# Optimization experiments

Hardware: AMD Instinct MI355X
Metric: run time of the kernel (lower is better)

The kernel has to match this reference:

```python
import jax, jax.numpy as jnp
import numpy as np

N, D, R, E = 20000, 256, 12, 200000  # nodes, feat dim, relation labels, edges


def setup_inputs() -> dict:
    key = jax.random.key(0)
    ks = jax.random.split(key, 8)
    x = jax.random.normal(ks[0], (N, D), dtype=jnp.float32)
    dep_idx = jax.random.randint(ks[1], (E,), 0, N)
    rel_idx = jax.random.randint(ks[2], (E,), 0, R)
    gov_idx = jax.random.randint(ks[3], (E,), 0, N)
    # nn.Linear params: W is [out,in], y = x @ W.T + b
    W_self = jax.random.normal(ks[4], (D, D), dtype=jnp.float32) * 0.02
    b_self = jnp.zeros((D,), dtype=jnp.float32)
    # 2R relation weights: [0..R) forward labels, [R..2R) reversed '_r' labels
    W_rel = jax.random.normal(ks[5], (2 * R, D, D), dtype=jnp.float32) * 0.02
    b_rel = jax.random.normal(ks[6], (2 * R, D), dtype=jnp.float32) * 0.02
    return {"x": x, "dep_idx": dep_idx, "rel_idx": rel_idx, "gov_idx": gov_idx,
            "W_self": W_self, "b_self": b_self, "W_rel": W_rel, "b_rel": b_rel}


def reference(x, dep_idx, rel_idx, gov_idx, W_self, b_self, W_rel, b_rel):
    R_ = W_rel.shape[0] // 2
    # self transform for every node
    out = x @ W_self.T + b_self  # [N, D]
    # all-relation transform, grouped GEMM instead of per-edge Linear calls
    T = jnp.einsum('nd,rod->nro', x, W_rel)  # [N, 2R, D]
    # forward edges: dependent += W[rel] @ x[governor] + b[rel]
    msg_f = T[gov_idx, rel_idx] + b_rel[rel_idx]          # [E, D]
    # reverse edges: governor += W[rel_r] @ x[dependent] + b[rel_r]
    msg_r = T[dep_idx, rel_idx + R_] + b_rel[rel_idx + R_]  # [E, D]
    out = out.at[dep_idx].add(msg_f).at[gov_idx].add(msg_r)
    return jax.nn.relu(out)
```

## Files before the change

### kernel.cpp

```cpp
#include <hip/hip_runtime.h>
#include <cstdint>
#include <cstddef>

#define DD 256
#define NSLOT 25
#define SELFSLOT 12

typedef unsigned short u16;
typedef __bf16 bf16t;
typedef bf16t bf16x8 __attribute__((ext_vector_type(8)));
typedef unsigned short us8 __attribute__((ext_vector_type(8)));
typedef unsigned short us4 __attribute__((ext_vector_type(4)));
typedef float f32x4 __attribute__((ext_vector_type(4)));

__device__ __forceinline__ u16 f2bf(float f) {
    uint32_t u = __builtin_bit_cast(uint32_t, f);
    u += 0x7FFFu + ((u >> 16) & 1u);
    return (u16)(u >> 16);
}
__device__ __forceinline__ float bf2f(u16 h) {
    uint32_t u = ((uint32_t)h) << 16;
    return __builtin_bit_cast(float, u);
}

__global__ void k_convert_all(const float* __restrict__ x, const float* __restrict__ W_rel,
                              const float* __restrict__ W_self, const float* __restrict__ b_self,
                              const float* __restrict__ b_rel,
                              u16* __restrict__ xb, u16* __restrict__ Wb,
                              float* __restrict__ ba, int NDD) {
    const int s0 = NDD;
    const int s1 = s0 + 12 * 65536;
    const int s2 = s1 + 65536;
    const int s3 = s2 + 12 * 65536;
    const int s4 = s3 + NSLOT * DD;
    int i = blockIdx.x * blockDim.x + threadIdx.x;
    int st = gridDim.x * blockDim.x;
    for (; i < s4; i += st) {
        if (i < s0) {
            xb[i] = f2bf(x[i]);
        } else if (i < s1) {
            int k = i - s0; Wb[k] = f2bf(W_rel[k]);
        } else if (i < s2) {
            int k = i - s1; Wb[12 * 65536 + k] = f2bf(W_self[k]);
        } else if (i < s3) {
            int k = i - s2; Wb[13 * 65536 + k] = f2bf(W_rel[12 * 65536 + k]);
        } else {
            int k = i - s3;
            float v;
            if (k < 12 * DD) v = b_rel[k];
            else if (k < 13 * DD) v = b_self[k - 12 * DD];
            else v = b_rel[k - DD];
            ba[k] = v;
        }
    }
}

__global__ void k_markhist(const int* __restrict__ dep, const int* __restrict__ rel,
                           const int* __restrict__ gov, int E, int N, int SG,
                           int* __restrict__ flag, int* __restrict__ bcnt) {
    int i = blockIdx.x * blockDim.x + threadIdx.x;
    int st = gridDim.x * blockDim.x;
    for (int j = i; j < E; j += st) {
        int r = rel[j], d = dep[j], g = gov[j];
        flag[r * N + g] = 1;
        flag[(13 + r) * N + d] = 1;
        atomicAdd(&bcnt[(r / SG) * N + d], 1);
        atomicAdd(&bcnt[((13 + r) / SG) * N + g], 1);
    }
    for (int j = i; j < N; j += st) flag[SELFSLOT * N + j] = 1;
}

__global__ void k_scan1d(const int* __restrict__ A, int* __restrict__ outA,
                         int* __restrict__ bsumA, int lenA, int nbA,
                         const int* __restrict__ B, int* __restrict__ outB,
                         int* __restrict__ bsumB, int lenB) {
    __shared__ int sm[256];
    const int* in; int* outp; int* bs; int len; int lb;
    if ((int)blockIdx.x < nbA) { in = A; outp = outA; bs = bsumA; len = lenA; lb = blockIdx.x; }
    else { in = B; outp = outB; bs = bsumB; len = lenB; lb = blockIdx.x - nbA; }
    int tid = threadIdx.x;
    int i = lb * 256 + tid;
    int v = (i < len) ? in[i] : 0;
    sm[tid] = v;
    __syncthreads();
    for (int off = 1; off < 256; off <<= 1) {
        int t = (tid >= off) ? sm[tid - off] : 0;
        __syncthreads();
        sm[tid] += t;
        __syncthreads();
    }
    if (i < len) outp[i] = sm[tid] - v;
    if (tid == 255) bs[lb] = sm[255];
}

__global__ void k_scan2d(const int* __restrict__ bsumA, int* __restrict__ bbasA, int nbA,
                         const int* __restrict__ bsumB, int* __restrict__ bbasB, int nbB) {
    __shared__ int sm[256];
    int t = threadIdx.x;
    for (int which = 0; which < 2; ++which) {
        const int* bsum = which ? bsumB : bsumA;
        int* bbase = which ? bbasB : bbasA;
        int nb = which ? nbB : nbA;
        int pre[8];
        int tot = 0;
        for (int j = 0; j < 8; ++j) {
            int idx = t * 8 + j;
            int v = (idx < nb) ? bsum[idx] : 0;
            pre[j] = tot;
            tot += v;
        }
        sm[t] = tot;
        __syncthreads();
        for (int off = 1; off < 256; off <<= 1) {
            int x = (t >= off) ? sm[t - off] : 0;
            __syncthreads();
            sm[t] += x;
            __syncthreads();
        }
        int base = sm[t] - tot;
        for (int j = 0; j < 8; ++j) {
            int idx = t * 8 + j;
            if (idx < nb) bbase[idx] = base + pre[j];
        }
        __syncthreads();
    }
}

__global__ void k_scan3d(int* __restrict__ pos, const int* __restrict__ bbasA,
                         const int* __restrict__ flag, int NN, int N,
                         int* __restrict__ rksrc,
                         int* __restrict__ bcsr, int* __restrict__ bcur,
                         const int* __restrict__ bbasB, int B2, int E2) {
    int i = blockIdx.x * 256 + threadIdx.x;
    if (i < NN) {
        int v = pos[i] + bbasA[i >> 8];
        pos[i] = v;
        if (i == NN - 1) pos[NN] = v + flag[i];
        if (flag[i]) {
            int slot = i / N;
            rksrc[v] = i - slot * N;
        }
    }
    if (i < B2) {
        int v = bcsr[i] + bbasB[i >> 8];
        bcsr[i] = v;
        bcur[i] = v;
    }
    if (i == 0) bcsr[B2] = E2;
}

__global__ void k_scatter(const int* __restrict__ dep, const int* __restrict__ rel,
                          const int* __restrict__ gov, int E, int N, int SG,
                          const int* __restrict__ pos,
                          int* __restrict__ cursor, int* __restrict__ epay) {
    int i = blockIdx.x * blockDim.x + threadIdx.x;
    int st = gridDim.x * blockDim.x;
    for (; i < E; i += st) {
        int r = rel[i], d = dep[i], g = gov[i];
        int g0 = r / SG;
        int p = atomicAdd(&cursor[g0 * N + d], 1);
        epay[p] = pos[r * N + g] - pos[g0 * SG * N];
        int gs = 13 + r;
        int g1 = gs / SG;
        int q = atomicAdd(&cursor[g1 * N + g], 1);
        epay[q] = pos[gs * N + d] - pos[g1 * SG * N];
    }
}

__global__ __launch_bounds__(256, 4) void k_T(
    const u16* __restrict__ xb, const u16* __restrict__ Wb, const float* __restrict__ ba,
    const int* __restrict__ pos, const int* __restrict__ rksrc, u16* __restrict__ T,
    int N, int gslot0, int Sg) {
    __shared__ u16 sm[2 * 128 * 72];
    __shared__ int s_src[128];
    u16 (*As)[72] = (u16(*)[72])sm;
    u16 (*Bs)[72] = (u16(*)[72])(sm + 128 * 72);

    const int bx = blockIdx.x;
    const int mtile = bx / (2 * Sg);
    const int rem = bx - mtile * 2 * Sg;
    const int slot = rem >> 1;
    const int n0 = (rem & 1) * 128;
    const int gslot = gslot0 + slot;
    const int u0 = pos[gslot * N];
    const int used = pos[(gslot + 1) * N] - u0;
    const int row0 = mtile * 128;
    if (row0 >= used) return;
    const int gbase = pos[gslot0 * N];
    const int tid = threadIdx.x;

    if (tid < 128) {
        int r = row0 + tid;
        s_src[tid] = rksrc[u0 + ((r < used) ? r : (used - 1))];
    }
    __syncthreads();

    const int lane = tid & 63, wv = tid >> 6;
    const int wr = wv & 1, wc = wv >> 1;
    const int l15 = lane & 15, quad = lane >> 4;
    const int srow = tid >> 1, sh = (tid & 1) * 32;
    const u16* bgp = Wb + ((size_t)gslot << 16) + (size_t)(n0 + srow) * DD + sh;

    f32x4 acc[4][4] = {};
    for (int kb = 0; kb < DD; kb += 64) {
        {
            const us8* ga = (const us8*)(xb + (size_t)s_src[srow] * DD + kb + sh);
            us8 a0 = ga[0], a1 = ga[1], a2 = ga[2], a3 = ga[3];
            *(us8*)&As[srow][sh]      = a0;
            *(us8*)&As[srow][sh + 8]  = a1;
            *(us8*)&As[srow][sh + 16] = a2;
            *(us8*)&As[srow][sh + 24] = a3;
            const us8* gb = (const us8*)(bgp + kb);
            us8 b0 = gb[0], b1 = gb[1], b2 = gb[2], b3 = gb[3];
            *(us8*)&Bs[srow][sh]      = b0;
            *(us8*)&Bs[srow][sh + 8]  = b1;
            *(us8*)&Bs[srow][sh + 16] = b2;
            *(us8*)&Bs[srow][sh + 24] = b3;
        }
        __syncthreads();
        #pragma unroll
        for (int ks = 0; ks < 2; ++ks) {
            const int kk = ks * 32 + quad * 8;
            bf16x8 af[4], bfv[4];
            #pragma unroll
            for (int mt = 0; mt < 4; ++mt)
                af[mt] = __builtin_bit_cast(bf16x8, *(const us8*)&As[wr * 64 + mt * 16 + l15][kk]);
            #pragma unroll
            for (int nt = 0; nt < 4; ++nt)
                bfv[nt] = __builtin_bit_cast(bf16x8, *(const us8*)&Bs[wc * 64 + nt * 16 + l15][kk]);
            #pragma unroll
            for (int mt = 0; mt < 4; ++mt)
                #pragma unroll
                for (int nt = 0; nt < 4; ++nt)
                    acc[mt][nt] = __builtin_amdgcn_mfma_f32_16x16x32_bf16(
                        af[mt], bfv[nt], acc[mt][nt], 0, 0, 0);
        }
        __syncthreads();
    }

    float bv[4];
    #pragma unroll
    for (int nt = 0; nt < 4; ++nt) bv[nt] = ba[gslot * DD + n0 + wc * 64 + nt * 16 + l15];
    u16* trb = sm + wv * (64 * 72);
    #pragma unroll
    for (int nt = 0; nt < 4; ++nt)
        #pragma unroll
        for (int mt = 0; mt < 4; ++mt)
            #pragma unroll
            for (int j = 0; j < 4; ++j)
                trb[(mt * 16 + quad * 4 + j) * 72 + nt * 16 + l15] =
                    f2bf(acc[mt][nt][j] + bv[nt]);
    __syncthreads();
    const int trow0 = u0 - gbase + row0 + wr * 64;
    const int half = lane & 1;
    #pragma unroll
    for (int it = 0; it < 2; ++it) {
        int r = it * 32 + (lane >> 1);
        if (row0 + wr * 64 + r < used) {
            const us8* sp = (const us8*)(trb + r * 72 + half * 32);
            us8 v0 = sp[0], v1 = sp[1], v2 = sp[2], v3 = sp[3];
            us8* dp = (us8*)(T + (size_t)(trow0 + r) * DD + n0 + wc * 64 + half * 32);
            dp[0] = v0; dp[1] = v1; dp[2] = v2; dp[3] = v3;
        }
    }
}

__global__ __launch_bounds__(256) void k_gather(
    const u16* __restrict__ T, const int* __restrict__ epay,
    const int* __restrict__ csr, const int* __restrict__ pos,
    float* __restrict__ out, int N, int bktBase, int selfKeyBase, int gfN,
    int first, int last) {
    int wid = (blockIdx.x * 256 + threadIdx.x) >> 6;
    if (wid >= N) return;
    int feat = (threadIdx.x & 63) * 4;
    f32x4 a = {0.0f, 0.0f, 0.0f, 0.0f};
    if (!first) a = *(const f32x4*)(out + (size_t)wid * DD + feat);
    if (selfKeyBase >= 0) {
        int p = pos[selfKeyBase + wid] - pos[gfN];
        us4 v = *(const us4*)(T + (size_t)p * DD + feat);
        a[0] += bf2f(v[0]); a[1] += bf2f(v[1]); a[2] += bf2f(v[2]); a[3] += bf2f(v[3]);
    }
    int beg = csr[bktBase + wid], end = csr[bktBase + wid + 1];
    f32x4 b = {0, 0, 0, 0}, c = {0, 0, 0, 0}, d4 = {0, 0, 0, 0};
    int j = beg;
    for (; j + 3 < end; j += 4) {
        int p0 = epay[j], p1 = epay[j + 1], p2 = epay[j + 2], p3 = epay[j + 3];
        us4 v0 = *(const us4*)(T + (size_t)p0 * DD + feat);
        us4 v1 = *(const us4*)(T + (size_t)p1 * DD + feat);
        us4 v2 = *(const us4*)(T + (size_t)p2 * DD + feat);
        us4 v3 = *(const us4*)(T + (size_t)p3 * DD + feat);
        a[0] += bf2f(v0[0]); a[1] += bf2f(v0[1]); a[2] += bf2f(v0[2]); a[3] += bf2f(v0[3]);
        b[0] += bf2f(v1[0]); b[1] += bf2f(v1[1]); b[2] += bf2f(v1[2]); b[3] += bf2f(v1[3]);
        c[0] += bf2f(v2[0]); c[1] += bf2f(v2[1]); c[2] += bf2f(v2[2]); c[3] += bf2f(v2[3]);
        d4[0] += bf2f(v3[0]); d4[1] += bf2f(v3[1]); d4[2] += bf2f(v3[2]); d4[3] += bf2f(v3[3]);
    }
    for (; j < end; ++j) {
        int p0 = epay[j];
        us4 v0 = *(const us4*)(T + (size_t)p0 * DD + feat);
        a[0] += bf2f(v0[0]); a[1] += bf2f(v0[1]); a[2] += bf2f(v0[2]); a[3] += bf2f(v0[3]);
    }
    a[0] += b[0] + c[0] + d4[0];
    a[1] += b[1] + c[1] + d4[1];
    a[2] += b[2] + c[2] + d4[2];
    a[3] += b[3] + c[3] + d4[3];
    if (last) {
        a[0] = fmaxf(a[0], 0.0f); a[1] = fmaxf(a[1], 0.0f);
        a[2] = fmaxf(a[2], 0.0f); a[3] = fmaxf(a[3], 0.0f);
    }
    *(f32x4*)(out + (size_t)wid * DD + feat) = a;
}

extern "C" void kernel_launch(void* const* d_in, const int* in_sizes, int n_in,
                              void* d_out, int out_size, void* d_ws, size_t ws_size,
                              hipStream_t stream) {
    const float* x      = (const float*)d_in[0];
    const int*   dep    = (const int*)  d_in[1];
    const int*   rel    = (const int*)  d_in[2];
    const int*   gov    = (const int*)  d_in[3];
    const float* W_self = (const float*)d_in[4];
    const float* b_self = (const float*)d_in[5];
    const float* W_rel  = (const float*)d_in[6];
    const float* b_rel  = (const float*)d_in[7];
    float* out = (float*)d_out;

    const int N  = in_sizes[0] / DD;
    const int E  = in_sizes[1];
    const int NN = NSLOT * N;

    char* w = (char*)d_ws;
    auto alloc = [&](size_t bytes) {
        char* p = w;
        w += (bytes + 255) & ~(size_t)255;
        return p;
    };
    u16* xb    = (u16*)alloc((size_t)N * DD * sizeof(u16));
    u16* Wb    = (u16*)alloc((size_t)NSLOT * DD * DD * sizeof(u16));
    float* ba  = (float*)alloc((size_t)NSLOT * DD * sizeof(float));
    int* flag  = (int*)alloc((size_t)NN * sizeof(int));
    int* pos   = (int*)alloc(((size_t)NN + 1) * sizeof(int));
    int* rksrc = (int*)alloc(((size_t)2 * E + N) * sizeof(int));
    int* bcnt  = (int*)alloc((size_t)6 * N * sizeof(int));
    int* bcsr  = (int*)alloc(((size_t)6 * N + 1) * sizeof(int));
    int* bcur  = (int*)alloc((size_t)6 * N * sizeof(int));
    int* bsumA = (int*)alloc((size_t)2048 * sizeof(int));
    int* bbasA = (int*)alloc((size_t)2048 * sizeof(int));
    int* bsumB = (int*)alloc((size_t)2048 * sizeof(int));
    int* bbasB = (int*)alloc((size_t)2048 * sizeof(int));
    int* epay  = (int*)alloc((size_t)2 * E * sizeof(int));

    size_t used = (size_t)(w - (char*)d_ws);
    size_t avail = (ws_size > used) ? (ws_size - used) : 0;

    int NGROUP = 2, SG = 13;
    for (int ng = 1; ng <= 5; ++ng) {
        int sg = (NSLOT + ng - 1) / ng;
        size_t maxB = 0;
        for (int g = 0; g < ng; ++g) {
            int s0 = g * sg, s1 = s0 + sg; if (s1 > NSLOT) s1 = NSLOT;
            if (s0 >= NSLOT) break;
            int hasSelf = (s0 <= SELFSLOT && SELFSLOT < s1) ? 1 : 0;
            size_t rels = (size_t)(s1 - s0 - hasSelf);
            size_t rows = rels * N; if (rows > (size_t)2 * E) rows = (size_t)2 * E;
            rows += hasSelf ? (size_t)N : 0;
            if (rows > maxB) maxB = rows;
        }
        if (maxB * ((size_t)DD * 2) <= avail) { NGROUP = ng; SG = sg; break; }
        NGROUP = ng + 1; SG = (NSLOT + NGROUP - 1) / NGROUP;
    }
    u16* T = (u16*)w;
    const int B2 = NGROUP * N;

    k_convert_all<<<1024, 256, 0, stream>>>(x, W_rel, W_self, b_self, b_rel,
                                            xb, Wb, ba, N * DD);

    hipMemsetAsync(flag, 0, (size_t)NN * sizeof(int), stream);
    hipMemsetAsync(bcnt, 0, (size_t)B2 * sizeof(int), stream);
    k_markhist<<<512, 256, 0, stream>>>(dep, rel, gov, E, N, SG, flag, bcnt);

    const int nbA = (NN + 255) / 256;
    const int nbB = (B2 + 255) / 256;
    k_scan1d<<<nbA + nbB, 256, 0, stream>>>(flag, pos, bsumA, NN, nbA, bcnt, bcsr, bsumB, B2);
    k_scan2d<<<1, 256, 0, stream>>>(bsumA, bbasA, nbA, bsumB, bbasB, nbB);
    k_scan3d<<<nbA, 256, 0, stream>>>(pos, bbasA, flag, NN, N, rksrc, bcsr, bcur, bbasB, B2, 2 * E);

    k_scatter<<<(E + 255) / 256, 256, 0, stream>>>(dep, rel, gov, E, N, SG, pos, bcur, epay);

    const int tilesPerSlot = (N + 127) / 128;
    const int gBlocks = (N + 3) / 4;
    for (int g = 0; g < NGROUP; ++g) {
        int s0 = g * SG;
        if (s0 >= NSLOT) break;
        int Sg = NSLOT - s0; if (Sg > SG) Sg = SG;
        k_T<<<dim3(tilesPerSlot * Sg * 2), 256, 0, stream>>>(
            xb, Wb, ba, pos, rksrc, T, N, s0, Sg);
        int hasSelf = (s0 <= SELFSLOT && SELFSLOT < s0 + Sg);
        k_gather<<<gBlocks, 256, 0, stream>>>(
            T, epay, bcsr, pos, out, N, g * N,
            hasSelf ? SELFSLOT * N : -1, s0 * N,
            (g == 0) ? 1 : 0, (g == NGROUP - 1) ? 1 : 0);
    }
}
```

Before: 279.3 us.

## Fuse convert and histogram kernels; transpose MFMA epilogue for vector stores

```diff
diff --git a/kernel.cpp b/kernel.cpp
--- a/kernel.cpp
+++ b/kernel.cpp
@@ -23,51 +23,51 @@
     return __builtin_bit_cast(float, u);
 }
 
-__global__ void k_convert_all(const float* __restrict__ x, const float* __restrict__ W_rel,
-                              const float* __restrict__ W_self, const float* __restrict__ b_self,
-                              const float* __restrict__ b_rel,
-                              u16* __restrict__ xb, u16* __restrict__ Wb,
-                              float* __restrict__ ba, int NDD) {
-    const int s0 = NDD;
-    const int s1 = s0 + 12 * 65536;
-    const int s2 = s1 + 65536;
-    const int s3 = s2 + 12 * 65536;
-    const int s4 = s3 + NSLOT * DD;
-    int i = blockIdx.x * blockDim.x + threadIdx.x;
-    int st = gridDim.x * blockDim.x;
-    for (; i < s4; i += st) {
-        if (i < s0) {
-            xb[i] = f2bf(x[i]);
-        } else if (i < s1) {
-            int k = i - s0; Wb[k] = f2bf(W_rel[k]);
-        } else if (i < s2) {
-            int k = i - s1; Wb[12 * 65536 + k] = f2bf(W_self[k]);
-        } else if (i < s3) {
-            int k = i - s2; Wb[13 * 65536 + k] = f2bf(W_rel[12 * 65536 + k]);
-        } else {
-            int k = i - s3;
-            float v;
-            if (k < 12 * DD) v = b_rel[k];
-            else if (k < 13 * DD) v = b_self[k - 12 * DD];
-            else v = b_rel[k - DD];
-            ba[k] = v;
-        }
-    }
-}
-
-__global__ void k_markhist(const int* __restrict__ dep, const int* __restrict__ rel,
-                           const int* __restrict__ gov, int E, int N, int SG,
-                           int* __restrict__ flag, int* __restrict__ bcnt) {
-    int i = blockIdx.x * blockDim.x + threadIdx.x;
-    int st = gridDim.x * blockDim.x;
-    for (int j = i; j < E; j += st) {
-        int r = rel[j], d = dep[j], g = gov[j];
-        flag[r * N + g] = 1;
-        flag[(13 + r) * N + d] = 1;
-        atomicAdd(&bcnt[(r / SG) * N + d], 1);
-        atomicAdd(&bcnt[((13 + r) / SG) * N + g], 1);
-    }
-    for (int j = i; j < N; j += st) flag[SELFSLOT * N + j] = 1;
+__global__ void k_prep(const float* __restrict__ x, const float* __restrict__ W_rel,
+                       const float* __restrict__ W_self, const float* __restrict__ b_self,
+                       const float* __restrict__ b_rel,
+                       u16* __restrict__ xb, u16* __restrict__ Wb, float* __restrict__ ba,
+                       const int* __restrict__ dep, const int* __restrict__ rel,
+                       const int* __restrict__ gov, int E, int N, int SG,
+                       int* __restrict__ flag, int* __restrict__ bcnt, int NDD) {
+    if (blockIdx.x < 1024) {
+        const int s0 = NDD;
+        const int s1 = s0 + 12 * 65536;
+        const int s2 = s1 + 65536;
+        const int s3 = s2 + 12 * 65536;
+        const int s4 = s3 + NSLOT * DD;
+        int i = blockIdx.x * 256 + threadIdx.x;
+        int st = 1024 * 256;
+        for (; i < s4; i += st) {
+            if (i < s0) {
+                xb[i] = f2bf(x[i]);
+            } else if (i < s1) {
+                int k = i - s0; Wb[k] = f2bf(W_rel[k]);
+            } else if (i < s2) {
+                int k = i - s1; Wb[12 * 65536 + k] = f2bf(W_self[k]);
+            } else if (i < s3) {
+                int k = i - s2; Wb[13 * 65536 + k] = f2bf(W_rel[12 * 65536 + k]);
+            } else {
+                int k = i - s3;
+                float v;
+                if (k < 12 * DD) v = b_rel[k];
+                else if (k < 13 * DD) v = b_self[k - 12 * DD];
+                else v = b_rel[k - DD];
+                ba[k] = v;
+            }
+        }
+    } else {
+        int i = (blockIdx.x - 1024) * 256 + threadIdx.x;
+        int st = 512 * 256;
+        for (int j = i; j < E; j += st) {
+            int r = rel[j], d = dep[j], g = gov[j];
+            flag[r * N + g] = 1;
+            flag[(13 + r) * N + d] = 1;
+            atomicAdd(&bcnt[(r / SG) * N + d], 1);
+            atomicAdd(&bcnt[((13 + r) / SG) * N + g], 1);
+        }
+        for (int j = i; j < N; j += st) flag[SELFSLOT * N + j] = 1;
+    }
 }
 
 __global__ void k_scan1d(const int* __restrict__ A, int* __restrict__ outA,
@@ -229,27 +229,29 @@
             for (int nt = 0; nt < 4; ++nt)
                 bfv[nt] = __builtin_bit_cast(bf16x8, *(const us8*)&Bs[wc * 64 + nt * 16 + l15][kk]);
             #pragma unroll
-            for (int mt = 0; mt < 4; ++mt)
+            for (int nt = 0; nt < 4; ++nt)
                 #pragma unroll
-                for (int nt = 0; nt < 4; ++nt)
-                    acc[mt][nt] = __builtin_amdgcn_mfma_f32_16x16x32_bf16(
-                        af[mt], bfv[nt], acc[mt][nt], 0, 0, 0);
-        }
-        __syncthreads();
-    }
-
-    float bv[4];
+                for (int mt = 0; mt < 4; ++mt)
+                    acc[nt][mt] = __builtin_amdgcn_mfma_f32_16x16x32_bf16(
+                        bfv[nt], af[mt], acc[nt][mt], 0, 0, 0);
+        }
+        __syncthreads();
+    }
+
+    f32x4 bb[4];
     #pragma unroll
-    for (int nt = 0; nt < 4; ++nt) bv[nt] = ba[gslot * DD + n0 + wc * 64 + nt * 16 + l15];
+    for (int nt = 0; nt < 4; ++nt)
+        bb[nt] = *(const f32x4*)(ba + gslot * DD + n0 + wc * 64 + nt * 16 + quad * 4);
     u16* trb = sm + wv * (64 * 72);
     #pragma unroll
-    for (int nt = 0; nt < 4; ++nt)
+    for (int mt = 0; mt < 4; ++mt)
         #pragma unroll
-        for (int mt = 0; mt < 4; ++mt)
+        for (int nt = 0; nt < 4; ++nt) {
+            us4 t4;
             #pragma unroll
-            for (int j = 0; j < 4; ++j)
-                trb[(mt * 16 + quad * 4 + j) * 72 + nt * 16 + l15] =
-                    f2bf(acc[mt][nt][j] + bv[nt]);
+            for (int j = 0; j < 4; ++j) t4[j] = f2bf(acc[nt][mt][j] + bb[nt][j]);
+            *(us4*)&trb[(size_t)(mt * 16 + l15) * 72 + nt * 16 + quad * 4] = t4;
+        }
     __syncthreads();
     const int trow0 = u0 - gbase + row0 + wr * 64;
     const int half = lane & 1;
@@ -260,7 +262,10 @@
             const us8* sp = (const us8*)(trb + r * 72 + half * 32);
             us8 v0 = sp[0], v1 = sp[1], v2 = sp[2], v3 = sp[3];
             us8* dp = (us8*)(T + (size_t)(trow0 + r) * DD + n0 + wc * 64 + half * 32);
-            dp[0] = v0; dp[1] = v1; dp[2] = v2; dp[3] = v3;
+            __builtin_nontemporal_store(v0, dp);
+            __builtin_nontemporal_store(v1, dp + 1);
+            __builtin_nontemporal_store(v2, dp + 2);
+            __builtin_nontemporal_store(v3, dp + 3);
         }
     }
 }
@@ -370,12 +375,10 @@
     u16* T = (u16*)w;
     const int B2 = NGROUP * N;
 
-    k_convert_all<<<1024, 256, 0, stream>>>(x, W_rel, W_self, b_self, b_rel,
-                                            xb, Wb, ba, N * DD);
-
     hipMemsetAsync(flag, 0, (size_t)NN * sizeof(int), stream);
     hipMemsetAsync(bcnt, 0, (size_t)B2 * sizeof(int), stream);
-    k_markhist<<<512, 256, 0, stream>>>(dep, rel, gov, E, N, SG, flag, bcnt);
+    k_prep<<<1536, 256, 0, stream>>>(x, W_rel, W_self, b_self, b_rel, xb, Wb, ba,
+                                     dep, rel, gov, E, N, SG, flag, bcnt, N * DD);
 
     const int nbA = (NN + 255) / 256;
     const int nbB = (B2 + 255) / 256;
```

New measurement: 407.5 us. 1.46x slower.
